# Kernel optimization log

Hardware: AMD Instinct MI355X
Metric: run time of the kernel (lower is better)

## Reference

```python
import jax, jax.numpy as jnp
import numpy as np

N = 100000       # nodes
E = 640000       # edges
G = 2048         # graphs in batch
IN_C, HID, NCLS = 3, 128, 4


def setup_inputs() -> dict:
    key = jax.random.key(0)
    ks = jax.random.split(key, 16)
    x = jax.random.normal(ks[0], (N, IN_C), dtype=jnp.float32)
    edge_index = jax.random.randint(ks[1], (2, E), 0, N, dtype=jnp.int64)
    batch = jnp.sort(jax.random.randint(ks[2], (N,), 0, G, dtype=jnp.int64))
    def glorot(k, shape):
        lim = np.sqrt(6.0 / (shape[0] + shape[1])).astype(np.float32)
        return jax.random.uniform(k, shape, jnp.float32, -lim, lim)
    return {
        "x": x, "edge_index": edge_index, "batch": batch,
        "W1": glorot(ks[3], (IN_C, HID)), "b1": jnp.zeros((HID,), jnp.float32),
        "W2": glorot(ks[4], (HID, HID)),  "b2": jnp.zeros((HID,), jnp.float32),
        "W3": glorot(ks[5], (HID, HID)),  "b3": jnp.zeros((HID,), jnp.float32),
        "W4": glorot(ks[6], (HID, HID)),  "b4": jnp.zeros((HID,), jnp.float32),
        "Wfc": glorot(ks[7], (HID, NCLS)), "bfc": jnp.zeros((NCLS,), jnp.float32),
    }


def _gcn_norm(edge_index):
    # Add self loops, then symmetric normalization D^{-1/2} (A+I) D^{-1/2}.
    loop = jnp.arange(N, dtype=edge_index.dtype)
    row = jnp.concatenate([edge_index[0], loop])  # source
    col = jnp.concatenate([edge_index[1], loop])  # target (aggregation side)
    deg = jax.ops.segment_sum(jnp.ones_like(col, dtype=jnp.float32), col,
                              num_segments=N)
    dinv = jnp.where(deg > 0, jax.lax.rsqrt(deg), 0.0)
    norm = dinv[row] * dinv[col]  # [E+N]
    return row, col, norm


def _gcn_layer(x, W, b, row, col, norm):
    h = x @ W                                 # [N, out]
    msg = h[row] * norm[:, None]              # gather + scale, [E+N, out]
    out = jax.ops.segment_sum(msg, col, num_segments=N)
    return out + b


def reference(x, edge_index, batch, W1, b1, W2, b2, W3, b3, W4, b4, Wfc, bfc):
    row, col, norm = _gcn_norm(edge_index)
    h = jax.nn.relu(_gcn_layer(x, W1, b1, row, col, norm))
    h = jax.nn.relu(_gcn_layer(h, W2, b2, row, col, norm))
    h = jax.nn.relu(_gcn_layer(h, W3, b3, row, col, norm))
    h = jax.nn.relu(_gcn_layer(h, W4, b4, row, col, norm))
    # global mean pool over graphs
    sums = jax.ops.segment_sum(h, batch, num_segments=G)           # [G, HID]
    cnt = jax.ops.segment_sum(jnp.ones((N,), jnp.float32), batch,
                              num_segments=G)
    pooled = sums / jnp.maximum(cnt, 1.0)[:, None]
    return pooled @ Wfc + bfc                                      # [G, NCLS]
```

## Files before the change

### kernel.cpp

```cpp
#include <hip/hip_runtime.h>
#include <hip/hip_bf16.h>

#define N_NODES  100000
#define N_EDGES  640000
#define N_GRAPHS 2048
#define HID      128
#define NB_SCAN  391
#define TILE     16
#define LDW      136

typedef _Float16 half_t;
typedef __attribute__((ext_vector_type(4))) _Float16 half4;
typedef __attribute__((ext_vector_type(8))) _Float16 half8;
typedef __attribute__((ext_vector_type(4))) float floatx4;

__global__ void k_prep(const int* __restrict__ col, int* __restrict__ deg,
                       const float* __restrict__ x, float4* __restrict__ xp,
                       half4* __restrict__ xh,
                       const float* __restrict__ W2, const float* __restrict__ W3,
                       const float* __restrict__ W4, half_t* __restrict__ Wt) {
    int idx = blockIdx.x * 256 + threadIdx.x;
    if (idx < N_EDGES) atomicAdd(&deg[col[idx]], 1);
    if (idx < N_NODES) {
        float x0 = x[idx * 3 + 0], x1 = x[idx * 3 + 1], x2 = x[idx * 3 + 2];
        xp[idx] = make_float4(x0, x1, x2, 0.f);
        half4 hv;
        hv.x = (half_t)x0; hv.y = (half_t)x1; hv.z = (half_t)x2; hv.w = (half_t)0.f;
        xh[idx] = hv;
    }
    if (idx < 3 * 128 * 128) {
        int l = idx >> 14;
        int e = idx & 16383;
        int cin = e >> 7, cout = e & 127;
        const float* W = (l == 0) ? W2 : ((l == 1) ? W3 : W4);
        Wt[l * 16384 + cout * 128 + cin] = (half_t)W[cin * 128 + cout];
    }
}

__global__ void k_scan1(const int* __restrict__ deg, int* __restrict__ row_ptr,
                        int* __restrict__ bsum, float* __restrict__ dinv) {
    __shared__ int s[256];
    int tid = threadIdx.x;
    int i = blockIdx.x * 256 + tid;
    int d = (i < N_NODES) ? deg[i] : 0;
    if (i < N_NODES) dinv[i] = rsqrtf((float)(d + 1));
    s[tid] = d;
    __syncthreads();
    for (int off = 1; off < 256; off <<= 1) {
        int v = (tid >= off) ? s[tid - off] : 0;
        __syncthreads();
        s[tid] += v;
        __syncthreads();
    }
    if (i < N_NODES) row_ptr[i] = s[tid] - d;
    if (tid == 255) bsum[blockIdx.x] = s[255];
}

__global__ void k_scan3(int* __restrict__ row_ptr, int* __restrict__ rp_work,
                        const int* __restrict__ bsum) {
    __shared__ int sred[256];
    int t = threadIdx.x, bid = blockIdx.x;
    int partial = 0;
    if (t < bid) partial += bsum[t];
    if (t + 256 < bid) partial += bsum[t + 256];
    sred[t] = partial;
    __syncthreads();
    for (int s = 128; s > 0; s >>= 1) {
        if (t < s) sred[t] += sred[t + s];
        __syncthreads();
    }
    int add = sred[0];
    int i = bid * 256 + t;
    if (i < N_NODES) {
        int v = row_ptr[i] + add;
        row_ptr[i] = v;
        rp_work[i] = v;
    }
    if (i == N_NODES) row_ptr[N_NODES] = N_EDGES;
}

__global__ void k_scatter(const int* __restrict__ row, const int* __restrict__ col,
                          int* __restrict__ rp_work,
                          const float* __restrict__ dinv, int2* __restrict__ epair) {
    int e = blockIdx.x * blockDim.x + threadIdx.x;
    if (e >= N_EDGES) return;
    int c = col[e];
    int r = row[e];
    int p = atomicAdd(&rp_work[c], 1);
    epair[p] = make_int2(r, __float_as_int(dinv[r] * dinv[c]));
}

__global__ __launch_bounds__(256) void k_aggx_fc1(const float4* __restrict__ xp,
                                                  const half4* __restrict__ xh,
                                                  const int* __restrict__ row_ptr,
                                                  const int2* __restrict__ epair,
                                                  const float* __restrict__ dinv,
                                                  const float* __restrict__ W1,
                                                  const float* __restrict__ b1,
                                                  half_t* __restrict__ h) {
    __shared__ float sax[256][3];
    int t = threadIdx.x;
    int nb = blockIdx.x * 256;
    int i = nb + t;
    if (i < N_NODES) {
        float di = dinv[i];
        float sw = di * di;
        float4 xv = xp[i];
        float a0 = sw * xv.x, a1 = sw * xv.y, a2 = sw * xv.z;
        int s = row_ptr[i], e = row_ptr[i + 1];
        int k = s;
        for (; k + 4 <= e; k += 4) {
            int2 pr[4];
#pragma unroll
            for (int r = 0; r < 4; r++) pr[r] = epair[k + r];
            half4 bx[4];
#pragma unroll
            for (int r = 0; r < 4; r++) bx[r] = xh[pr[r].x];
#pragma unroll
            for (int r = 0; r < 4; r++) {
                float w = __int_as_float(pr[r].y);
                a0 += w * (float)bx[r].x;
                a1 += w * (float)bx[r].y;
                a2 += w * (float)bx[r].z;
            }
        }
        for (; k < e; k++) {
            int2 pr = epair[k];
            float w = __int_as_float(pr.y);
            half4 bx = xh[pr.x];
            a0 += w * (float)bx.x;
            a1 += w * (float)bx.y;
            a2 += w * (float)bx.z;
        }
        sax[t][0] = a0; sax[t][1] = a1; sax[t][2] = a2;
    }
    __syncthreads();
    int cq = t & 31, g8 = t >> 5;
    const float4* W14 = (const float4*)W1;
    float4 w0 = W14[cq], w1 = W14[32 + cq], w2 = W14[64 + cq];
    float4 bb = ((const float4*)b1)[cq];
    for (int pass = 0; pass < 32; pass++) {
        int local = pass * 8 + g8;
        int node = nb + local;
        if (node >= N_NODES) break;
        float x0 = sax[local][0], x1 = sax[local][1], x2 = sax[local][2];
        half4 o;
        o.x = (half_t)fmaxf(bb.x + x0 * w0.x + x1 * w1.x + x2 * w2.x, 0.f);
        o.y = (half_t)fmaxf(bb.y + x0 * w0.y + x1 * w1.y + x2 * w2.y, 0.f);
        o.z = (half_t)fmaxf(bb.z + x0 * w0.z + x1 * w1.z + x2 * w2.z, 0.f);
        o.w = (half_t)fmaxf(bb.w + x0 * w0.w + x1 * w1.w + x2 * w2.w, 0.f);
        ((half4*)h)[(size_t)node * 32 + cq] = o;
    }
}

__global__ __launch_bounds__(256, 8) void k_agg_mm(const half_t* __restrict__ h_in,
                                                   const int* __restrict__ row_ptr,
                                                   const int2* __restrict__ epair,
                                                   const float* __restrict__ dinv,
                                                   const half_t* __restrict__ Wt,
                                                   const float* __restrict__ b,
                                                   half_t* __restrict__ h_out) {
    __shared__ __align__(16) half_t gs[TILE][LDW];
    int tid = threadIdx.x;
    int n0 = blockIdx.x * TILE;
    int lane16 = tid & 15;
    int gidx = tid >> 4;
    const half8* h8 = (const half8*)h_in;

    {
        int i = n0 + gidx;
        float di = dinv[i];
        float sw = di * di;
        half8 v = h8[(size_t)i * 16 + lane16];
        float acc[8];
#pragma unroll
        for (int c = 0; c < 8; c++) acc[c] = sw * (float)v[c];
        int s = row_ptr[i], e = row_ptr[i + 1];
        if (s < e) {
            int em1 = e - 1;
            int2 p0 = epair[s];
            int k1 = min(s + 1, em1);
            int2 p1 = epair[k1];
            float w0 = __int_as_float(p0.y);
            float w1 = (s + 1 < e) ? __int_as_float(p1.y) : 0.f;
            half8 u0 = h8[(size_t)p0.x * 16 + lane16];
            half8 u1 = h8[(size_t)p1.x * 16 + lane16];
            for (int k = s; k < e; k += 2) {
                int k2 = min(k + 2, em1);
                int k3 = min(k + 3, em1);
                int2 p2 = epair[k2];
                int2 p3 = epair[k3];
                float w2 = (k + 2 < e) ? __int_as_float(p2.y) : 0.f;
                float w3 = (k + 3 < e) ? __int_as_float(p3.y) : 0.f;
                half8 m0 = h8[(size_t)p2.x * 16 + lane16];
                half8 m1 = h8[(size_t)p3.x * 16 + lane16];
#pragma unroll
                for (int c = 0; c < 8; c++) acc[c] += w0 * (float)u0[c] + w1 * (float)u1[c];
                u0 = m0; u1 = m1; w0 = w2; w1 = w3;
            }
        }
        half8 av;
#pragma unroll
        for (int c = 0; c < 8; c++) av[c] = (half_t)acc[c];
        *(half8*)(&gs[gidx][lane16 * 8]) = av;
    }
    __syncthreads();

    int wv = tid >> 6;
    int ln = tid & 15;
    int q  = (tid >> 4) & 3;
    int cbase = wv * 32;
    floatx4 C[2];
#pragma unroll
    for (int t = 0; t < 2; t++) {
        float bn = b[cbase + t * 16 + ln];
        C[t].x = bn; C[t].y = bn; C[t].z = bn; C[t].w = bn;
    }
#pragma unroll
    for (int kq = 0; kq < 4; kq++) {
        half8 a = *(const half8*)(&gs[ln][kq * 32 + q * 8]);
#pragma unroll
        for (int t = 0; t < 2; t++) {
            half8 bf = *(const half8*)(Wt + (size_t)(cbase + t * 16 + ln) * 128 + kq * 32 + q * 8);
            C[t] = __builtin_amdgcn_mfma_f32_16x16x32_f16(a, bf, C[t], 0, 0, 0);
        }
    }

    __syncthreads();
#pragma unroll
    for (int t = 0; t < 2; t++) {
#pragma unroll
        for (int reg = 0; reg < 4; reg++) {
            float dv = (reg == 0) ? C[t].x : (reg == 1) ? C[t].y : (reg == 2) ? C[t].z : C[t].w;
            gs[q * 4 + reg][cbase + t * 16 + ln] = (half_t)fmaxf(dv, 0.f);
        }
    }
    __syncthreads();
    {
        int r0 = tid >> 4;
        int c0 = tid & 15;
        int4* dst = (int4*)(h_out + (size_t)(n0 + r0) * 128);
        const int4* srcp = (const int4*)(&gs[r0][0]);
        dst[c0] = srcp[c0];
    }
}

__global__ __launch_bounds__(128) void k_pool_final(const half_t* __restrict__ h,
                                                    const int* __restrict__ batch,
                                                    const float* __restrict__ Wfc,
                                                    const float* __restrict__ bfc,
                                                    float* __restrict__ out) {
    __shared__ float sred[8][128];
    __shared__ float red[128][4];
    __shared__ int sb_s, eb_s;
    int g = blockIdx.x, t = threadIdx.x;
    if (t == 0) {
        int lo = 0, hi = N_NODES;
        while (lo < hi) { int mid = (lo + hi) >> 1; if (batch[mid] < g) lo = mid + 1; else hi = mid; }
        sb_s = lo;
        hi = N_NODES;
        while (lo < hi) { int mid = (lo + hi) >> 1; if (batch[mid] < g + 1) lo = mid + 1; else hi = mid; }
        eb_s = lo;
    }
    __syncthreads();
    int sb = sb_s, eb = eb_s;
    int lane16 = t & 15, slot = t >> 4;
    const half8* h8 = (const half8*)h;
    float acc[8];
#pragma unroll
    for (int c = 0; c < 8; c++) acc[c] = 0.f;
    for (int n = sb + slot; n < eb; n += 8) {
        half8 v = h8[(size_t)n * 16 + lane16];
#pragma unroll
        for (int c = 0; c < 8; c++) acc[c] += (float)v[c];
    }
#pragma unroll
    for (int c = 0; c < 8; c++) sred[slot][lane16 * 8 + c] = acc[c];
    __syncthreads();
    float pv = 0.f;
#pragma unroll
    for (int s2 = 0; s2 < 8; s2++) pv += sred[s2][t];
    float inv = 1.0f / fmaxf((float)(eb - sb), 1.0f);
    float v = pv * inv;
    float4 w = ((const float4*)Wfc)[t];
    red[t][0] = v * w.x; red[t][1] = v * w.y; red[t][2] = v * w.z; red[t][3] = v * w.w;
    __syncthreads();
    for (int s = 64; s > 0; s >>= 1) {
        if (t < s) {
            red[t][0] += red[t + s][0];
            red[t][1] += red[t + s][1];
            red[t][2] += red[t + s][2];
            red[t][3] += red[t + s][3];
        }
        __syncthreads();
    }
    if (t < 4) out[g * 4 + t] = red[0][t] + bfc[t];
}

extern "C" void kernel_launch(void* const* d_in, const int* in_sizes, int n_in,
                              void* d_out, int out_size, void* d_ws, size_t ws_size,
                              hipStream_t stream) {
    const float* x     = (const float*)d_in[0];
    const int*   ei    = (const int*)d_in[1];
    const int*   row   = ei;
    const int*   col   = ei + N_EDGES;
    const int*   batch = (const int*)d_in[2];
    const float* W1 = (const float*)d_in[3];
    const float* b1 = (const float*)d_in[4];
    const float* W2 = (const float*)d_in[5];
    const float* b2 = (const float*)d_in[6];
    const float* W3 = (const float*)d_in[7];
    const float* b3 = (const float*)d_in[8];
    const float* W4 = (const float*)d_in[9];
    const float* b4 = (const float*)d_in[10];
    const float* Wfc = (const float*)d_in[11];
    const float* bfc = (const float*)d_in[12];
    float* out = (float*)d_out;

    char* ws = (char*)d_ws;
    size_t off = 0;
    auto take = [&](size_t bytes) -> char* {
        char* p = ws + off;
        off = (off + bytes + 255) & ~(size_t)255;
        return p;
    };
    int*    deg     = (int*)take(N_NODES * 4);
    int*    row_ptr = (int*)take((N_NODES + 1) * 4);
    int*    rp_work = (int*)take(N_NODES * 4);
    int*    bsum    = (int*)take(512 * 4);
    float*  dinv    = (float*)take(N_NODES * 4);
    float4* xp      = (float4*)take((size_t)N_NODES * 16);
    half4*  xh      = (half4*)take((size_t)N_NODES * 8);
    int2*   epair   = (int2*)take((size_t)N_EDGES * 8);
    half_t* wt16    = (half_t*)take((size_t)3 * 128 * 128 * 2);
    half_t* bufA    = (half_t*)take((size_t)N_NODES * 128 * 2);
    half_t* bufB    = (half_t*)take((size_t)N_NODES * 128 * 2);

    hipMemsetAsync(deg, 0, N_NODES * 4, stream);

    k_prep<<<(N_EDGES + 255) / 256, 256, 0, stream>>>(col, deg, x, xp, xh, W2, W3, W4, wt16);
    k_scan1<<<NB_SCAN, 256, 0, stream>>>(deg, row_ptr, bsum, dinv);
    k_scan3<<<NB_SCAN, 256, 0, stream>>>(row_ptr, rp_work, bsum);
    k_scatter<<<(N_EDGES + 255) / 256, 256, 0, stream>>>(row, col, rp_work, dinv, epair);
    k_aggx_fc1<<<NB_SCAN, 256, 0, stream>>>(xp, xh, row_ptr, epair, dinv, W1, b1, bufA);

    const int NBF = N_NODES / TILE;
    k_agg_mm<<<NBF, 256, 0, stream>>>(bufA, row_ptr, epair, dinv, wt16,         b2, bufB);
    k_agg_mm<<<NBF, 256, 0, stream>>>(bufB, row_ptr, epair, dinv, wt16 + 16384, b3, bufA);
    k_agg_mm<<<NBF, 256, 0, stream>>>(bufA, row_ptr, epair, dinv, wt16 + 32768, b4, bufB);

    k_pool_final<<<N_GRAPHS, 128, 0, stream>>>(bufB, batch, Wfc, bfc, out);
}
```

Measured before the change: 314.1 us.

## Bin nodes by degree within chunks to balance aggregation tiles

Adds a kernel that counting-sorts nodes by in-degree (capped at 32 bins) inside chunks of 2048 nodes, producing a permutation. The aggregation+MFMA kernels then process 16 permuted nodes per tile and scatter results back to their original rows. The goal is to cut load imbalance, since the 16 node-groups in a tile would otherwise wait on the highest-degree node. The cost is an extra kernel, an indirect lookup per node, and scattered output writes and input reads that lose contiguity.

```diff
diff --git a/kernel.cpp b/kernel.cpp
--- a/kernel.cpp
+++ b/kernel.cpp
@@ -8,6 +8,9 @@
 #define NB_SCAN  391
 #define TILE     16
 #define LDW      136
+#define NBIN     32
+#define CHUNK    2048
+#define NCHUNK   49
 
 typedef _Float16 half_t;
 typedef __attribute__((ext_vector_type(4))) _Float16 half4;
@@ -77,6 +80,52 @@
         rp_work[i] = v;
     }
     if (i == N_NODES) row_ptr[N_NODES] = N_EDGES;
+}
+
+__global__ __launch_bounds__(256) void k_lperm(const int* __restrict__ deg,
+                                               int* __restrict__ perm) {
+    __shared__ int cnt[NBIN][256];
+    __shared__ int base[NBIN];
+    int t = threadIdx.x;
+    int c0 = blockIdx.x * CHUNK;
+#pragma unroll
+    for (int b = 0; b < NBIN; b++) cnt[b][t] = 0;
+    __syncthreads();
+    int mybin[8];
+#pragma unroll
+    for (int j = 0; j < 8; j++) {
+        int i = c0 + t * 8 + j;
+        mybin[j] = -1;
+        if (i < N_NODES) {
+            int bin = min(deg[i], NBIN - 1);
+            mybin[j] = bin;
+            cnt[bin][t]++;
+        }
+    }
+    __syncthreads();
+    if (t < NBIN) {
+        int run = 0;
+        for (int tt = 0; tt < 256; tt++) {
+            int v = cnt[t][tt];
+            cnt[t][tt] = run;
+            run += v;
+        }
+        base[t] = run;
+    }
+    __syncthreads();
+    if (t == 0) {
+        int run = 0;
+        for (int b = 0; b < NBIN; b++) { int v = base[b]; base[b] = run; run += v; }
+    }
+    __syncthreads();
+#pragma unroll
+    for (int j = 0; j < 8; j++) {
+        if (mybin[j] >= 0) {
+            int bin = mybin[j];
+            int rank = cnt[bin][t]++;
+            perm[c0 + base[bin] + rank] = c0 + t * 8 + j;
+        }
+    }
 }
 
 __global__ void k_scatter(const int* __restrict__ row, const int* __restrict__ col,
@@ -157,6 +206,7 @@
                                                    const int* __restrict__ row_ptr,
                                                    const int2* __restrict__ epair,
                                                    const float* __restrict__ dinv,
+                                                   const int* __restrict__ perm,
                                                    const half_t* __restrict__ Wt,
                                                    const float* __restrict__ b,
                                                    half_t* __restrict__ h_out) {
@@ -168,14 +218,14 @@
     const half8* h8 = (const half8*)h_in;
 
     {
-        int i = n0 + gidx;
-        float di = dinv[i];
+        int node = perm[n0 + gidx];
+        float di = dinv[node];
         float sw = di * di;
-        half8 v = h8[(size_t)i * 16 + lane16];
+        half8 v = h8[(size_t)node * 16 + lane16];
         float acc[8];
 #pragma unroll
         for (int c = 0; c < 8; c++) acc[c] = sw * (float)v[c];
-        int s = row_ptr[i], e = row_ptr[i + 1];
+        int s = row_ptr[node], e = row_ptr[node + 1];
         if (s < e) {
             int em1 = e - 1;
             int2 p0 = epair[s];
@@ -239,7 +289,8 @@
     {
         int r0 = tid >> 4;
         int c0 = tid & 15;
-        int4* dst = (int4*)(h_out + (size_t)(n0 + r0) * 128);
+        int pn = perm[n0 + r0];
+        int4* dst = (int4*)(h_out + (size_t)pn * 128);
         const int4* srcp = (const int4*)(&gs[r0][0]);
         dst[c0] = srcp[c0];
     }
@@ -329,6 +380,7 @@
     int*    rp_work = (int*)take(N_NODES * 4);
     int*    bsum    = (int*)take(512 * 4);
     float*  dinv    = (float*)take(N_NODES * 4);
+    int*    perm    = (int*)take(N_NODES * 4);
     float4* xp      = (float4*)take((size_t)N_NODES * 16);
     half4*  xh      = (half4*)take((size_t)N_NODES * 8);
     int2*   epair   = (int2*)take((size_t)N_EDGES * 8);
@@ -341,13 +393,14 @@
     k_prep<<<(N_EDGES + 255) / 256, 256, 0, stream>>>(col, deg, x, xp, xh, W2, W3, W4, wt16);
     k_scan1<<<NB_SCAN, 256, 0, stream>>>(deg, row_ptr, bsum, dinv);
     k_scan3<<<NB_SCAN, 256, 0, stream>>>(row_ptr, rp_work, bsum);
+    k_lperm<<<NCHUNK, 256, 0, stream>>>(deg, perm);
     k_scatter<<<(N_EDGES + 255) / 256, 256, 0, stream>>>(row, col, rp_work, dinv, epair);
     k_aggx_fc1<<<NB_SCAN, 256, 0, stream>>>(xp, xh, row_ptr, epair, dinv, W1, b1, bufA);
 
     const int NBF = N_NODES / TILE;
-    k_agg_mm<<<NBF, 256, 0, stream>>>(bufA, row_ptr, epair, dinv, wt16,         b2, bufB);
-    k_agg_mm<<<NBF, 256, 0, stream>>>(bufB, row_ptr, epair, dinv, wt16 + 16384, b3, bufA);
-    k_agg_mm<<<NBF, 256, 0, stream>>>(bufA, row_ptr, epair, dinv, wt16 + 32768, b4, bufB);
+    k_agg_mm<<<NBF, 256, 0, stream>>>(bufA, row_ptr, epair, dinv, perm, wt16,         b2, bufB);
+    k_agg_mm<<<NBF, 256, 0, stream>>>(bufB, row_ptr, epair, dinv, perm, wt16 + 16384, b3, bufA);
+    k_agg_mm<<<NBF, 256, 0, stream>>>(bufA, row_ptr, epair, dinv, perm, wt16 + 32768, b4, bufB);
 
     k_pool_final<<<N_GRAPHS, 128, 0, stream>>>(bufB, batch, Wfc, bfc, out);
 }
```

Measured after the change: 314.1 us. Within noise of the previous version (-0.0%).
